# Kernel optimization log

Measured on AMD Instinct MI355X. Metric: run time of the kernel, lower is better.

Reference implementation:

```python
import jax, jax.numpy as jnp
import numpy as np

# dims: B nodes, K hops, N neighbors/node, channels/features per FeatTrans1d stage
B, K, N = 512, 2, 32
C0, F0 = 1, 512
C1, F1 = 4, 16
C2, F2 = 32, 1
NUM_CLASS = 40
EPS_BN = 1e-5
EPS_NORM = 1e-7


def softsign(x):
    return x / (1.0 + jnp.abs(x))


def sgnroot(x):
    return jnp.sign(x) * jnp.sqrt(jnp.abs(x))


def row_normalize(x):
    # normalize over axis 1 as in the torch code; NaN -> 0
    x = x / (jnp.abs(x).sum(axis=1, keepdims=True) + EPS_NORM)
    return jnp.where(jnp.isnan(x), 0.0, x)


def feature_adjacency(x, nb):
    # x: [B,C,F], nb: [B,N,C,F] -> fadj: [B,F,F]
    fadj = jnp.einsum('bcf,bncg->bfg', x, nb)
    fadj = fadj + jnp.swapaxes(fadj, -1, -2)
    return row_normalize(sgnroot(fadj))


def transform(x, fadj, W):
    # x: [B,C,F], fadj: [B,F,G], W: [D,C,G,E] -> [B,D,E]
    xg = jnp.einsum('bcf,bfg->bcg', x, fadj)
    return jnp.einsum('bcg,dcge->bde', xg, W)


def transform_nb(nb, fadj, W):
    # nb: [B,N,C,F], fadj: [B,F,G] (node i's fadj broadcast over its N neighbors)
    xg = jnp.einsum('bncf,bfg->bncg', nb, fadj)
    return jnp.einsum('bncg,dcge->bnde', xg, W)


def bn(x, gamma, beta, axes, ch_axis):
    # training-mode BatchNorm1d: batch stats per channel (biased variance)
    mean = x.mean(axes, keepdims=True)
    var = x.var(axes, keepdims=True)
    shape = [1] * x.ndim
    shape[ch_axis] = x.shape[ch_axis]
    return (x - mean) * jax.lax.rsqrt(var + EPS_BN) * gamma.reshape(shape) + beta.reshape(shape)


def setup_inputs() -> dict:
    key = jax.random.key(0)
    ks = jax.random.split(key, 8)
    x = jax.random.normal(ks[0], (B, C0, F0), jnp.float32)
    neighbor = jax.random.normal(ks[1], (B, K, N, C0, F0), jnp.float32)
    W1 = jax.random.normal(ks[2], (K, C1, C0, F0, F1), jnp.float32) * 0.05
    W2 = jax.random.normal(ks[3], (K, C2, C1, F1, F2), jnp.float32) * 0.1
    g1 = jnp.ones((K, C1), jnp.float32)
    b1 = jnp.zeros((K, C1), jnp.float32)
    g2 = jnp.ones((K, C2), jnp.float32)
    b2 = jnp.zeros((K, C2), jnp.float32)
    Wc1 = jax.random.normal(ks[4], (C2 * F2 * K, C2 * F2), jnp.float32) * 0.1
    bc1 = jnp.zeros((C2 * F2,), jnp.float32)
    Wc2 = jax.random.normal(ks[5], (C2 * F2, NUM_CLASS), jnp.float32) * 0.1
    bc2 = jnp.zeros((NUM_CLASS,), jnp.float32)
    return {"x": x, "neighbor": neighbor, "W1": W1, "g1": g1, "b1": b1,
            "W2": W2, "g2": g2, "b2": b2,
            "Wc1": Wc1, "bc1": bc1, "Wc2": Wc2, "bc2": bc2}


def reference(x, neighbor, W1, g1, b1, W2, g2, b2, Wc1, bc1, Wc2, bc2):
    outs = []
    for kk in range(K):  # fixed small hop count, structurally distinct weights
        nb_k = neighbor[:, kk]                      # [B,N,C0,F0]
        fadj1 = feature_adjacency(x, nb_k)          # [B,F0,F0]
        h = transform(x, fadj1, W1[kk])             # [B,C1,F1]
        nbh = transform_nb(nb_k, fadj1, W1[kk])     # [B,N,C1,F1]
        # BN over batch+feature dims for h; per-node BN over (N,F) for neighbors
        h = softsign(bn(h, g1[kk], b1[kk], (0, 2), 1))
        nbh = softsign(bn(nbh, g1[kk], b1[kk], (1, 3), 2))
        fadj2 = feature_adjacency(h, nbh)           # [B,F1,F1]
        h2 = transform(h, fadj2, W2[kk])            # [B,C2,F2]
        h2 = softsign(bn(h2, g2[kk], b2[kk], (0, 2), 1))
        outs.append(h2)
    x_khops = jnp.concatenate(outs, axis=1)         # [B, C2*K, F2]
    flat = x_khops.reshape(B, -1)                   # dropout is identity at eval
    hid = jax.nn.relu(flat @ Wc1 + bc1)
    return hid @ Wc2 + bc2                          # [B, NUM_CLASS]
```

## Files before the change

### kernel.cpp

```cpp
#include <hip/hip_runtime.h>
#include <hip/hip_bf16.h>

#define B_SZ 512
#define KHOP 2
#define NNB  32
#define F0   512
#define C1   4
#define F1   16
#define C2   32
#define NCLS 40

#define EPS_BN   1e-5f
#define EPS_NORM 1e-7f

typedef __attribute__((ext_vector_type(8))) short short8;
typedef __attribute__((ext_vector_type(4))) float f32x4;

__device__ __forceinline__ float softsignf(float v) { return v / (1.0f + fabsf(v)); }

__device__ __forceinline__ unsigned cvt_pk_bf16(float lo, float hi) {
    unsigned r;
    asm("v_cvt_pk_bf16_f32 %0, %1, %2" : "=v"(r) : "v"(lo), "v"(hi));
    return r;
}

#define SMEM_MAIN 74752

__global__ __launch_bounds__(256, 2) void k_main(
    const float* __restrict__ xg_, const float* __restrict__ nbg,
    const float* __restrict__ W1,
    const float* __restrict__ g1, const float* __restrict__ b1,
    float* __restrict__ h_raw, float* __restrict__ nbs_out,
    float* __restrict__ hsum)
{
    extern __shared__ char smem[];
    float* xl   = (float*)(smem + 65536);
    float* sl   = (float*)(smem + 67584);
    float* invD = (float*)(smem + 69632);
    float* xgx  = (float*)(smem + 71680);
    float* redh = (float*)(smem + 73728);

    const int t = threadIdx.x;
    const int pair = blockIdx.x;
    const int b = pair >> 1, k = pair & 1;
    const int l = t & 63, w = t >> 6;

    {
        const int oct = t & 63, ng = t >> 6;
        const int f0s = oct * 8;
        const float* nbp = nbg + (size_t)pair * (NNB * F0);
        float sp0=0,sp1=0,sp2=0,sp3=0,sp4=0,sp5=0,sp6=0,sp7=0;
        #pragma unroll
        for (int ni = 0; ni < 8; ++ni) {
            const int n = ng * 8 + ni;
            float4 q0 = *(const float4*)(nbp + n * F0 + f0s);
            float4 q1 = *(const float4*)(nbp + n * F0 + f0s + 4);
            sp0 += q0.x; sp1 += q0.y; sp2 += q0.z; sp3 += q0.w;
            sp4 += q1.x; sp5 += q1.y; sp6 += q1.z; sp7 += q1.w;
            uint4 p;
            p.x = cvt_pk_bf16(q0.x, q0.y);
            p.y = cvt_pk_bf16(q0.z, q0.w);
            p.z = cvt_pk_bf16(q1.x, q1.y);
            p.w = cvt_pk_bf16(q1.z, q1.w);
            *(uint4*)(smem + n * 1024 + ((2 * f0s) ^ ((n & 7) << 4))) = p;
        }
        float* part = (float*)(smem + 32768);
        *(float4*)(part + ng * 512 + f0s)     = make_float4(sp0, sp1, sp2, sp3);
        *(float4*)(part + ng * 512 + f0s + 4) = make_float4(sp4, sp5, sp6, sp7);
        xl[t]       = xg_[b * F0 + t];
        xl[t + 256] = xg_[b * F0 + t + 256];
    }
    __syncthreads();
    {
        const float* part = (const float*)(smem + 32768);
        float sA = part[t] + part[512 + t] + part[1024 + t] + part[1536 + t];
        float sB = part[t + 256] + part[512 + t + 256]
                 + part[1024 + t + 256] + part[1536 + t + 256];
        sl[t] = sA; sl[t + 256] = sB;
    }
    __syncthreads();

    const int gA = t, gB = t + 256;
    const float xa = xl[gA], xb = xl[gB];
    const float sa = sl[gA], sb = sl[gB];
    float dA0=0.f, dA1=0.f, dB0=0.f, dB1=0.f;
    float xA0=0.f, xA1=0.f, xB0=0.f, xB1=0.f;

    f32x4 acc[2][8];
    #pragma unroll
    for (int m = 0; m < 2; ++m)
        #pragma unroll
        for (int j = 0; j < 8; ++j)
            acc[m][j] = (f32x4){0.f, 0.f, 0.f, 0.f};

    const int swA = ((gA >> 1) & 3) << 4;
    const int swB = ((gB >> 1) & 3) << 4;
    const int kol = l >> 4;

    #pragma unroll 1
    for (int strip = 0; strip < 16; ++strip) {
        const int f0 = strip * 32;
        #pragma unroll
        for (int ko = 0; ko < 4; ++ko) {
            float4 xf0 = ((const float4*)xl)[(f0 >> 2) + ko * 2];
            float4 xf1 = ((const float4*)xl)[(f0 >> 2) + ko * 2 + 1];
            float4 sf0 = ((const float4*)sl)[(f0 >> 2) + ko * 2];
            float4 sf1 = ((const float4*)sl)[(f0 >> 2) + ko * 2 + 1];
            const float xf[8] = {xf0.x, xf0.y, xf0.z, xf0.w, xf1.x, xf1.y, xf1.z, xf1.w};
            const float sf[8] = {sf0.x, sf0.y, sf0.z, sf0.w, sf1.x, sf1.y, sf1.z, sf1.w};
            uint pa[4], pb[4];
            float vpA = 0.f, vpB = 0.f;
            #pragma unroll
            for (int i = 0; i < 8; ++i) {
                float rA = xf[i] * sa + xa * sf[i];
                float aA = sqrtf(fabsf(rA));
                float vA = copysignf(aA, rA);
                float rB = xf[i] * sb + xb * sf[i];
                float aB = sqrtf(fabsf(rB));
                float vB = copysignf(aB, rB);
                if (i & 1) {
                    dA1 += aA; dB1 += aB; xA1 += xf[i] * vA; xB1 += xf[i] * vB;
                    pa[i >> 1] = cvt_pk_bf16(vpA, vA);
                    pb[i >> 1] = cvt_pk_bf16(vpB, vB);
                } else {
                    dA0 += aA; dB0 += aB; xA0 += xf[i] * vA; xB0 += xf[i] * vB;
                    vpA = vA; vpB = vB;
                }
            }
            uint4 ua; ua.x = pa[0]; ua.y = pa[1]; ua.z = pa[2]; ua.w = pa[3];
            uint4 ub; ub.x = pb[0]; ub.y = pb[1]; ub.z = pb[2]; ub.w = pb[3];
            *(uint4*)(smem + 32768 + gA * 64 + ((ko * 16) ^ swA)) = ua;
            *(uint4*)(smem + 32768 + gB * 64 + ((ko * 16) ^ swB)) = ub;
        }
        __syncthreads();
        short8 afrag[2];
        #pragma unroll
        for (int m = 0; m < 2; ++m) {
            const int n = m * 16 + (l & 15);
            afrag[m] = *(const short8*)(smem + n * 1024 +
                        ((f0 * 2 + kol * 16) ^ ((n & 7) << 4)));
        }
        #pragma unroll
        for (int j = 0; j < 8; ++j) {
            const int g = w * 128 + j * 16 + (l & 15);
            short8 bfrag = *(const short8*)(smem + 32768 + g * 64 +
                            ((kol * 16) ^ (((g >> 1) & 3) << 4)));
            acc[0][j] = __builtin_amdgcn_mfma_f32_16x16x32_bf16(afrag[0], bfrag, acc[0][j], 0, 0, 0);
            acc[1][j] = __builtin_amdgcn_mfma_f32_16x16x32_bf16(afrag[1], bfrag, acc[1][j], 0, 0, 0);
        }
        __syncthreads();
    }

    {
        const float ia = 1.f / ((dA0 + dA1) + EPS_NORM);
        const float ib = 1.f / ((dB0 + dB1) + EPS_NORM);
        invD[gA] = ia; xgx[gA] = (xA0 + xA1) * ia;
        invD[gB] = ib; xgx[gB] = (xB0 + xB1) * ib;
    }
    __syncthreads();

    #pragma unroll
    for (int m = 0; m < 2; ++m)
        #pragma unroll
        for (int j = 0; j < 8; ++j) {
            const int g = w * 128 + j * 16 + (l & 15);
            const float iv = invD[g];
            #pragma unroll
            for (int r = 0; r < 4; ++r) {
                const int n = m * 16 + (l >> 4) * 4 + r;
                unsigned pv = cvt_pk_bf16(acc[m][j][r] * iv, 0.f);
                *(unsigned short*)(smem + n * 1024 + ((2 * g) ^ ((n & 7) << 4))) =
                    (unsigned short)pv;
            }
        }
    __syncthreads();

    f32x4 acc3[2];
    acc3[0] = (f32x4){0.f, 0.f, 0.f, 0.f};
    acc3[1] = (f32x4){0.f, 0.f, 0.f, 0.f};
    {
        const int de = w * 16 + (l & 15);
        const int d3 = de >> 4, e3 = de & 15;
        const float* Wp3 = W1 + ((k * 4 + d3) * 512) * 16 + e3;
        #pragma unroll 2
        for (int ks = 0; ks < 16; ++ks) {
            const int gg0 = ks * 32 + kol * 8;
            float w0 = Wp3[(gg0 + 0) * 16], w1 = Wp3[(gg0 + 1) * 16];
            float w2 = Wp3[(gg0 + 2) * 16], w3 = Wp3[(gg0 + 3) * 16];
            float w4 = Wp3[(gg0 + 4) * 16], w5 = Wp3[(gg0 + 5) * 16];
            float w6 = Wp3[(gg0 + 6) * 16], w7 = Wp3[(gg0 + 7) * 16];
            uint4 bp;
            bp.x = cvt_pk_bf16(w0, w1); bp.y = cvt_pk_bf16(w2, w3);
            bp.z = cvt_pk_bf16(w4, w5); bp.w = cvt_pk_bf16(w6, w7);
            short8 bfrag;
            __builtin_memcpy(&bfrag, &bp, 16);
            #pragma unroll
            for (int m = 0; m < 2; ++m) {
                const int n = m * 16 + (l & 15);
                short8 af = *(const short8*)(smem + n * 1024 +
                            ((ks * 64 + kol * 16) ^ ((n & 7) << 4)));
                acc3[m] = __builtin_amdgcn_mfma_f32_16x16x32_bf16(af, bfrag, acc3[m], 0, 0, 0);
            }
        }
    }

    {
        float vals[8];
        float s1 = 0.f, s2 = 0.f;
        #pragma unroll
        for (int m = 0; m < 2; ++m)
            #pragma unroll
            for (int r = 0; r < 4; ++r) {
                float v = acc3[m][r];
                vals[m * 4 + r] = v; s1 += v; s2 += v * v;
            }
        #pragma unroll
        for (int off = 32; off >= 1; off >>= 1) {
            s1 += __shfl_xor(s1, off);
            s2 += __shfl_xor(s2, off);
        }
        const float mean = s1 * (1.f / 512.f);
        const float var  = s2 * (1.f / 512.f) - mean * mean;
        const float An   = g1[k * C1 + w] * rsqrtf(var + EPS_BN);
        const float Bn   = b1[k * C1 + w] - mean * An;
        float nbse = 0.f;
        #pragma unroll
        for (int i = 0; i < 8; ++i) nbse += softsignf(vals[i] * An + Bn);
        nbse += __shfl_xor(nbse, 16);
        nbse += __shfl_xor(nbse, 32);
        if (l < 16) nbs_out[pair * 64 + w * 16 + l] = nbse;
    }

    {
        const int de2 = t & 63, gs = t >> 6;
        const int d = de2 >> 4, e = de2 & 15;
        const float* Wp = W1 + ((k * 4 + d) * 512) * 16 + e;
        float a0 = 0.f, a1 = 0.f;
        const int gbeg = gs * 128;
        #pragma unroll 8
        for (int gi = 0; gi < 128; gi += 2) {
            a0 += xgx[gbeg + gi]     * Wp[(gbeg + gi) * 16];
            a1 += xgx[gbeg + gi + 1] * Wp[(gbeg + gi + 1) * 16];
        }
        redh[gs * 64 + de2] = a0 + a1;
    }
    __syncthreads();
    if (t < 64) {
        float hv = redh[t] + redh[64 + t] + redh[128 + t] + redh[192 + t];
        h_raw[pair * 64 + t] = hv;
        float s1 = hv, s2 = hv * hv;
        #pragma unroll
        for (int off = 1; off <= 8; off <<= 1) {
            s1 += __shfl_xor(s1, off);
            s2 += __shfl_xor(s2, off);
        }
        if ((t & 15) == 0) {
            atomicAdd(&hsum[k * 4 + (t >> 4)], s1);
            atomicAdd(&hsum[8 + k * 4 + (t >> 4)], s2);
        }
    }
}

__global__ __launch_bounds__(256) void k_stage2(
    const float* __restrict__ h_rawg, const float* __restrict__ nbsg,
    const float* __restrict__ hsum,
    const float* __restrict__ g1, const float* __restrict__ b1,
    const float* __restrict__ W2,
    float* __restrict__ h2_raw, float* __restrict__ h2sum)
{
    __shared__ float hl[4][64], nl[4][64], fl[4][256], xg2l[4][64];
    const int t = threadIdx.x, wv = t >> 6, l = t & 63;
    const int pair = blockIdx.x * 4 + wv;
    const int k = pair & 1;
    const int d = l >> 4;
    {
        const float S1 = hsum[k * 4 + d], S2 = hsum[8 + k * 4 + d];
        const float mean = S1 * (1.f / 8192.f);
        const float var  = S2 * (1.f / 8192.f) - mean * mean;
        const float A = g1[k * 4 + d] * rsqrtf(var + EPS_BN);
        const float Bc = b1[k * 4 + d] - mean * A;
        float hv = h_rawg[pair * 64 + l];
        hl[wv][l] = softsignf(hv * A + Bc);
        nl[wv][l] = nbsg[pair * 64 + l];
    }
    __syncthreads();
    const int gcol = l & 15;
    float raw[4];
    #pragma unroll
    for (int j = 0; j < 4; ++j) {
        const int idx = l + 64 * j;
        const int f = idx >> 4;
        float a = 0.f;
        #pragma unroll
        for (int c = 0; c < 4; ++c) a += hl[wv][c * 16 + f] * nl[wv][c * 16 + gcol];
        raw[j] = a;
        fl[wv][idx] = a;
    }
    __syncthreads();
    float w4[4]; float Dp = 0.f;
    #pragma unroll
    for (int j = 0; j < 4; ++j) {
        const int idx = l + 64 * j;
        const int f = idx >> 4;
        float v = raw[j] + fl[wv][gcol * 16 + f];
        float a = sqrtf(fabsf(v));
        Dp += a;
        w4[j] = copysignf(a, v);
    }
    Dp += __shfl_xor(Dp, 16);
    Dp += __shfl_xor(Dp, 32);
    const float invD = 1.f / (Dp + EPS_NORM);
    __syncthreads();
    #pragma unroll
    for (int j = 0; j < 4; ++j) fl[wv][l + 64 * j] = w4[j] * invD;
    __syncthreads();
    {
        const int c = l >> 4;
        float a = 0.f;
        #pragma unroll
        for (int f = 0; f < 16; ++f) a += hl[wv][c * 16 + f] * fl[wv][f * 16 + gcol];
        xg2l[wv][c * 16 + gcol] = a;
    }
    __syncthreads();
    if (l < 32) {
        const float* W2p = W2 + k * (C2 * C1 * F1) + l * (C1 * F1);
        float a = 0.f;
        #pragma unroll
        for (int i = 0; i < 64; ++i) a += xg2l[wv][i] * W2p[i];
        h2_raw[pair * 32 + l] = a;
        atomicAdd(&h2sum[k * 32 + l], a);
        atomicAdd(&h2sum[64 + k * 32 + l], a * a);
    }
}

__global__ __launch_bounds__(64) void k_cls(
    const float* __restrict__ h2_raw, const float* __restrict__ h2sum,
    const float* __restrict__ g2, const float* __restrict__ b2,
    const float* __restrict__ Wc1, const float* __restrict__ bc1,
    const float* __restrict__ Wc2, const float* __restrict__ bc2,
    float* __restrict__ out)
{
    __shared__ float flat[64];
    __shared__ float hid[32];
    const int b = blockIdx.x, l = threadIdx.x;
    const int k = l >> 5, d = l & 31;
    {
        const float S1 = h2sum[l], S2 = h2sum[64 + l];
        const float mean = S1 * (1.f / 512.f);
        const float var  = S2 * (1.f / 512.f) - mean * mean;
        const float A = g2[l] * rsqrtf(var + EPS_BN);
        const float Bc = b2[l] - mean * A;
        float v = h2_raw[(b * 2 + k) * 32 + d];
        flat[l] = softsignf(v * A + Bc);
    }
    __syncthreads();
    if (l < 32) {
        float a = bc1[l];
        #pragma unroll
        for (int i = 0; i < 64; ++i) a += flat[i] * Wc1[i * 32 + l];
        hid[l] = fmaxf(a, 0.f);
    }
    __syncthreads();
    if (l < NCLS) {
        float a = bc2[l];
        #pragma unroll
        for (int j = 0; j < 32; ++j) a += hid[j] * Wc2[j * NCLS + l];
        out[b * NCLS + l] = a;
    }
}

extern "C" void kernel_launch(void* const* d_in, const int* in_sizes, int n_in,
                              void* d_out, int out_size, void* d_ws, size_t ws_size,
                              hipStream_t stream)
{
    const float* x   = (const float*)d_in[0];
    const float* nbg = (const float*)d_in[1];
    const float* W1  = (const float*)d_in[2];
    const float* g1  = (const float*)d_in[3];
    const float* b1  = (const float*)d_in[4];
    const float* W2  = (const float*)d_in[5];
    const float* g2  = (const float*)d_in[6];
    const float* b2  = (const float*)d_in[7];
    const float* Wc1 = (const float*)d_in[8];
    const float* bc1 = (const float*)d_in[9];
    const float* Wc2 = (const float*)d_in[10];
    const float* bc2 = (const float*)d_in[11];
    float* out = (float*)d_out;
    float* ws  = (float*)d_ws;

    float* h_raw  = ws;
    float* nbs    = ws + 65536;
    float* h2_raw = ws + 131072;
    float* stats  = ws + 163840;
    float* hsum   = stats;
    float* h2sum  = stats + 16;

    hipMemsetAsync(stats, 0, 144 * sizeof(float), stream);
    hipLaunchKernelGGL(k_main,   dim3(B_SZ * KHOP),     dim3(256), SMEM_MAIN, stream,
                       x, nbg, W1, g1, b1, h_raw, nbs, hsum);
    hipLaunchKernelGGL(k_stage2, dim3(B_SZ * KHOP / 4), dim3(256), 0, stream,
                       h_raw, nbs, hsum, g1, b1, W2, h2_raw, h2sum);
    hipLaunchKernelGGL(k_cls,    dim3(B_SZ),            dim3(64), 0, stream,
                       h2_raw, h2sum, g2, b2, Wc1, bc1, Wc2, bc2, out);
}
```

Before: 305.6 us.

## Stream neighbor A-fragments from global, pre-transpose W1 to bf16, fold h into MFMA

The 32KB shared-memory copy of the neighbor matrix is dropped. Each strip now loads its A fragments straight from global memory, which cuts LDS use so three blocks can fit per CU instead of two. A new prep kernel writes W1 transposed to bf16 once per call, so the W1 MFMA stage reads contiguous short8 fragments instead of doing strided fp32 loads and converts. The h projection is computed as an extra MFMA with a single-row A fragment, which removes the scalar reduction and one barrier. The cost is re-reading neighbor data from global or cache each strip, bf16 precision for h, and reusing the h2_raw workspace for w1t before k_stage2 overwrites it.

```diff
diff --git a/kernel.cpp b/kernel.cpp
--- a/kernel.cpp
+++ b/kernel.cpp
@@ -24,31 +24,39 @@
     return r;
 }
 
-#define SMEM_MAIN 74752
-
-__global__ __launch_bounds__(256, 2) void k_main(
+__global__ __launch_bounds__(256) void k_prep(const float* __restrict__ W1,
+                                              unsigned short* __restrict__ w1t)
+{
+    const int idx = blockIdx.x * 256 + threadIdx.x;
+    const int g  = idx & 511;
+    const int de = (idx >> 9) & 63;
+    const int kk = idx >> 15;
+    const int d = de >> 4, e = de & 15;
+    w1t[idx] = (unsigned short)cvt_pk_bf16(W1[((size_t)((kk * 4 + d) * 512) + g) * 16 + e], 0.f);
+}
+
+#define SMEM_MAIN 36864
+
+__global__ __launch_bounds__(256, 3) void k_main(
     const float* __restrict__ xg_, const float* __restrict__ nbg,
-    const float* __restrict__ W1,
+    const unsigned short* __restrict__ w1t,
     const float* __restrict__ g1, const float* __restrict__ b1,
     float* __restrict__ h_raw, float* __restrict__ nbs_out,
     float* __restrict__ hsum)
 {
     extern __shared__ char smem[];
-    float* xl   = (float*)(smem + 65536);
-    float* sl   = (float*)(smem + 67584);
-    float* invD = (float*)(smem + 69632);
-    float* xgx  = (float*)(smem + 71680);
-    float* redh = (float*)(smem + 73728);
+    float* xl = (float*)(smem + 32768);
+    float* sl = (float*)(smem + 34816);
 
     const int t = threadIdx.x;
     const int pair = blockIdx.x;
     const int b = pair >> 1, k = pair & 1;
     const int l = t & 63, w = t >> 6;
+    const float* nbp = nbg + (size_t)pair * (NNB * F0);
 
     {
         const int oct = t & 63, ng = t >> 6;
         const int f0s = oct * 8;
-        const float* nbp = nbg + (size_t)pair * (NNB * F0);
         float sp0=0,sp1=0,sp2=0,sp3=0,sp4=0,sp5=0,sp6=0,sp7=0;
         #pragma unroll
         for (int ni = 0; ni < 8; ++ni) {
@@ -57,14 +65,8 @@
             float4 q1 = *(const float4*)(nbp + n * F0 + f0s + 4);
             sp0 += q0.x; sp1 += q0.y; sp2 += q0.z; sp3 += q0.w;
             sp4 += q1.x; sp5 += q1.y; sp6 += q1.z; sp7 += q1.w;
-            uint4 p;
-            p.x = cvt_pk_bf16(q0.x, q0.y);
-            p.y = cvt_pk_bf16(q0.z, q0.w);
-            p.z = cvt_pk_bf16(q1.x, q1.y);
-            p.w = cvt_pk_bf16(q1.z, q1.w);
-            *(uint4*)(smem + n * 1024 + ((2 * f0s) ^ ((n & 7) << 4))) = p;
-        }
-        float* part = (float*)(smem + 32768);
+        }
+        float* part = (float*)smem;
         *(float4*)(part + ng * 512 + f0s)     = make_float4(sp0, sp1, sp2, sp3);
         *(float4*)(part + ng * 512 + f0s + 4) = make_float4(sp4, sp5, sp6, sp7);
         xl[t]       = xg_[b * F0 + t];
@@ -72,11 +74,10 @@
     }
     __syncthreads();
     {
-        const float* part = (const float*)(smem + 32768);
-        float sA = part[t] + part[512 + t] + part[1024 + t] + part[1536 + t];
-        float sB = part[t + 256] + part[512 + t + 256]
-                 + part[1024 + t + 256] + part[1536 + t + 256];
-        sl[t] = sA; sl[t + 256] = sB;
+        const float* part = (const float*)smem;
+        sl[t]       = part[t] + part[512 + t] + part[1024 + t] + part[1536 + t];
+        sl[t + 256] = part[t + 256] + part[512 + t + 256]
+                    + part[1024 + t + 256] + part[1536 + t + 256];
     }
     __syncthreads();
 
@@ -96,10 +97,17 @@
     const int swA = ((gA >> 1) & 3) << 4;
     const int swB = ((gB >> 1) & 3) << 4;
     const int kol = l >> 4;
+    const float* aptr0 = nbp + (l & 15) * F0 + kol * 8;
+    const float* aptr1 = nbp + (16 + (l & 15)) * F0 + kol * 8;
 
     #pragma unroll 1
     for (int strip = 0; strip < 16; ++strip) {
         const int f0 = strip * 32;
+        float4 a00 = *(const float4*)(aptr0 + f0);
+        float4 a01 = *(const float4*)(aptr0 + f0 + 4);
+        float4 a10 = *(const float4*)(aptr1 + f0);
+        float4 a11 = *(const float4*)(aptr1 + f0 + 4);
+
         #pragma unroll
         for (int ko = 0; ko < 4; ++ko) {
             float4 xf0 = ((const float4*)xl)[(f0 >> 2) + ko * 2];
@@ -108,7 +116,7 @@
             float4 sf1 = ((const float4*)sl)[(f0 >> 2) + ko * 2 + 1];
             const float xf[8] = {xf0.x, xf0.y, xf0.z, xf0.w, xf1.x, xf1.y, xf1.z, xf1.w};
             const float sf[8] = {sf0.x, sf0.y, sf0.z, sf0.w, sf1.x, sf1.y, sf1.z, sf1.w};
-            uint pa[4], pb[4];
+            unsigned pa[4], pb[4];
             float vpA = 0.f, vpB = 0.f;
             #pragma unroll
             for (int i = 0; i < 8; ++i) {
@@ -129,21 +137,25 @@
             }
             uint4 ua; ua.x = pa[0]; ua.y = pa[1]; ua.z = pa[2]; ua.w = pa[3];
             uint4 ub; ub.x = pb[0]; ub.y = pb[1]; ub.z = pb[2]; ub.w = pb[3];
-            *(uint4*)(smem + 32768 + gA * 64 + ((ko * 16) ^ swA)) = ua;
-            *(uint4*)(smem + 32768 + gB * 64 + ((ko * 16) ^ swB)) = ub;
+            *(uint4*)(smem + gA * 64 + ((ko * 16) ^ swA)) = ua;
+            *(uint4*)(smem + gB * 64 + ((ko * 16) ^ swB)) = ub;
         }
         __syncthreads();
+
         short8 afrag[2];
-        #pragma unroll
-        for (int m = 0; m < 2; ++m) {
-            const int n = m * 16 + (l & 15);
-            afrag[m] = *(const short8*)(smem + n * 1024 +
-                        ((f0 * 2 + kol * 16) ^ ((n & 7) << 4)));
+        {
+            uint4 p0, p1;
+            p0.x = cvt_pk_bf16(a00.x, a00.y); p0.y = cvt_pk_bf16(a00.z, a00.w);
+            p0.z = cvt_pk_bf16(a01.x, a01.y); p0.w = cvt_pk_bf16(a01.z, a01.w);
+            p1.x = cvt_pk_bf16(a10.x, a10.y); p1.y = cvt_pk_bf16(a10.z, a10.w);
+            p1.z = cvt_pk_bf16(a11.x, a11.y); p1.w = cvt_pk_bf16(a11.z, a11.w);
+            __builtin_memcpy(&afrag[0], &p0, 16);
+            __builtin_memcpy(&afrag[1], &p1, 16);
         }
         #pragma unroll
         for (int j = 0; j < 8; ++j) {
             const int g = w * 128 + j * 16 + (l & 15);
-            short8 bfrag = *(const short8*)(smem + 32768 + g * 64 +
+            short8 bfrag = *(const short8*)(smem + g * 64 +
                             ((kol * 16) ^ (((g >> 1) & 3) << 4)));
             acc[0][j] = __builtin_amdgcn_mfma_f32_16x16x32_bf16(afrag[0], bfrag, acc[0][j], 0, 0, 0);
             acc[1][j] = __builtin_amdgcn_mfma_f32_16x16x32_bf16(afrag[1], bfrag, acc[1][j], 0, 0, 0);
@@ -154,46 +166,51 @@
     {
         const float ia = 1.f / ((dA0 + dA1) + EPS_NORM);
         const float ib = 1.f / ((dB0 + dB1) + EPS_NORM);
-        invD[gA] = ia; xgx[gA] = (xA0 + xA1) * ia;
-        invD[gB] = ib; xgx[gB] = (xB0 + xB1) * ib;
-    }
-    __syncthreads();
-
-    #pragma unroll
-    for (int m = 0; m < 2; ++m)
-        #pragma unroll
-        for (int j = 0; j < 8; ++j) {
-            const int g = w * 128 + j * 16 + (l & 15);
-            const float iv = invD[g];
+        sl[gA] = ia; sl[gB] = ib;
+        xl[gA] = (xA0 + xA1) * ia;
+        xl[gB] = (xB0 + xB1) * ib;
+    }
+    __syncthreads();
+
+    {
+        float iv[8];
+        #pragma unroll
+        for (int j = 0; j < 8; ++j) iv[j] = sl[w * 128 + j * 16 + (l & 15)];
+        #pragma unroll
+        for (int m = 0; m < 2; ++m)
             #pragma unroll
-            for (int r = 0; r < 4; ++r) {
-                const int n = m * 16 + (l >> 4) * 4 + r;
-                unsigned pv = cvt_pk_bf16(acc[m][j][r] * iv, 0.f);
-                *(unsigned short*)(smem + n * 1024 + ((2 * g) ^ ((n & 7) << 4))) =
-                    (unsigned short)pv;
+            for (int j = 0; j < 8; ++j) {
+                const int g = w * 128 + j * 16 + (l & 15);
+                #pragma unroll
+                for (int r = 0; r < 4; ++r) {
+                    const int n = m * 16 + (l >> 4) * 4 + r;
+                    *(unsigned short*)(smem + n * 1024 + ((2 * g) ^ ((n & 7) << 4))) =
+                        (unsigned short)cvt_pk_bf16(acc[m][j][r] * iv[j], 0.f);
+                }
             }
-        }
+    }
     __syncthreads();
 
     f32x4 acc3[2];
     acc3[0] = (f32x4){0.f, 0.f, 0.f, 0.f};
     acc3[1] = (f32x4){0.f, 0.f, 0.f, 0.f};
+    f32x4 acch = (f32x4){0.f, 0.f, 0.f, 0.f};
     {
         const int de = w * 16 + (l & 15);
-        const int d3 = de >> 4, e3 = de & 15;
-        const float* Wp3 = W1 + ((k * 4 + d3) * 512) * 16 + e3;
+        const unsigned short* wtp = w1t + ((size_t)(k * 64 + de) * 512) + kol * 8;
+        const float* xgx = xl;
         #pragma unroll 2
         for (int ks = 0; ks < 16; ++ks) {
-            const int gg0 = ks * 32 + kol * 8;
-            float w0 = Wp3[(gg0 + 0) * 16], w1 = Wp3[(gg0 + 1) * 16];
-            float w2 = Wp3[(gg0 + 2) * 16], w3 = Wp3[(gg0 + 3) * 16];
-            float w4 = Wp3[(gg0 + 4) * 16], w5 = Wp3[(gg0 + 5) * 16];
-            float w6 = Wp3[(gg0 + 6) * 16], w7 = Wp3[(gg0 + 7) * 16];
-            uint4 bp;
-            bp.x = cvt_pk_bf16(w0, w1); bp.y = cvt_pk_bf16(w2, w3);
-            bp.z = cvt_pk_bf16(w4, w5); bp.w = cvt_pk_bf16(w6, w7);
-            short8 bfrag;
-            __builtin_memcpy(&bfrag, &bp, 16);
+            short8 bfrag = *(const short8*)(wtp + ks * 32);
+            short8 afh = {0, 0, 0, 0, 0, 0, 0, 0};
+            if ((l & 15) == 0) {
+                float4 p0 = *(const float4*)(xgx + ks * 32 + kol * 8);
+                float4 p1 = *(const float4*)(xgx + ks * 32 + kol * 8 + 4);
+                uint4 pk;
+                pk.x = cvt_pk_bf16(p0.x, p0.y); pk.y = cvt_pk_bf16(p0.z, p0.w);
+                pk.z = cvt_pk_bf16(p1.x, p1.y); pk.w = cvt_pk_bf16(p1.z, p1.w);
+                __builtin_memcpy(&afh, &pk, 16);
+            }
             #pragma unroll
             for (int m = 0; m < 2; ++m) {
                 const int n = m * 16 + (l & 15);
@@ -201,6 +218,7 @@
                             ((ks * 64 + kol * 16) ^ ((n & 7) << 4)));
                 acc3[m] = __builtin_amdgcn_mfma_f32_16x16x32_bf16(af, bfrag, acc3[m], 0, 0, 0);
             }
+            acch = __builtin_amdgcn_mfma_f32_16x16x32_bf16(afh, bfrag, acch, 0, 0, 0);
         }
     }
 
@@ -231,32 +249,18 @@
         if (l < 16) nbs_out[pair * 64 + w * 16 + l] = nbse;
     }
 
-    {
-        const int de2 = t & 63, gs = t >> 6;
-        const int d = de2 >> 4, e = de2 & 15;
-        const float* Wp = W1 + ((k * 4 + d) * 512) * 16 + e;
-        float a0 = 0.f, a1 = 0.f;
-        const int gbeg = gs * 128;
-        #pragma unroll 8
-        for (int gi = 0; gi < 128; gi += 2) {
-            a0 += xgx[gbeg + gi]     * Wp[(gbeg + gi) * 16];
-            a1 += xgx[gbeg + gi + 1] * Wp[(gbeg + gi + 1) * 16];
-        }
-        redh[gs * 64 + de2] = a0 + a1;
-    }
-    __syncthreads();
-    if (t < 64) {
-        float hv = redh[t] + redh[64 + t] + redh[128 + t] + redh[192 + t];
-        h_raw[pair * 64 + t] = hv;
+    if (l < 16) {
+        float hv = acch[0];
+        h_raw[pair * 64 + w * 16 + l] = hv;
         float s1 = hv, s2 = hv * hv;
         #pragma unroll
         for (int off = 1; off <= 8; off <<= 1) {
             s1 += __shfl_xor(s1, off);
             s2 += __shfl_xor(s2, off);
         }
-        if ((t & 15) == 0) {
-            atomicAdd(&hsum[k * 4 + (t >> 4)], s1);
-            atomicAdd(&hsum[8 + k * 4 + (t >> 4)], s2);
+        if (l == 0) {
+            atomicAdd(&hsum[k * 4 + w], s1);
+            atomicAdd(&hsum[8 + k * 4 + w], s2);
         }
     }
 }
@@ -394,10 +398,12 @@
     float* stats  = ws + 163840;
     float* hsum   = stats;
     float* h2sum  = stats + 16;
+    unsigned short* w1t = (unsigned short*)h2_raw;
 
     hipMemsetAsync(stats, 0, 144 * sizeof(float), stream);
+    hipLaunchKernelGGL(k_prep,   dim3(256),             dim3(256), 0, stream, W1, w1t);
     hipLaunchKernelGGL(k_main,   dim3(B_SZ * KHOP),     dim3(256), SMEM_MAIN, stream,
-                       x, nbg, W1, g1, b1, h_raw, nbs, hsum);
+                       x, nbg, w1t, g1, b1, h_raw, nbs, hsum);
     hipLaunchKernelGGL(k_stage2, dim3(B_SZ * KHOP / 4), dim3(256), 0, stream,
                        h_raw, nbs, hsum, g1, b1, W2, h2_raw, h2sum);
     hipLaunchKernelGGL(k_cls,    dim3(B_SZ),            dim3(64), 0, stream,
```

Result: slower. 330.1 us (+8.0%).
